# Kernel optimization log

Measured on AMD Instinct MI355X. Metric: run time of the kernel, lower is better.

The kernel has to match this reference:

```python
import jax, jax.numpy as jnp
import numpy as np

B, S, D, H = 1, 2048, 1024, 16
HD = D // H
DFF = 4 * D
EPS = 1e-5


def _layernorm(x, g, b):
    mu = jnp.mean(x, axis=-1, keepdims=True)
    var = jnp.mean(jnp.square(x - mu), axis=-1, keepdims=True)
    return (x - mu) * jax.lax.rsqrt(var + EPS) * g + b


def setup_inputs() -> dict:
    key = jax.random.key(0)
    ks = jax.random.split(key, 8)
    scale = 1.0 / np.sqrt(D)
    # standard ALiBi slopes: 2^(-8*i/H)
    slopes = jnp.asarray(2.0 ** (-8.0 * (np.arange(1, H + 1) / H)), dtype=jnp.float32)
    return {
        "x": jax.random.normal(ks[0], (B, S, D), jnp.float32),
        "alibi_slopes": slopes,
        "wq": jax.random.normal(ks[1], (D, D), jnp.float32) * scale,
        "wk": jax.random.normal(ks[2], (D, D), jnp.float32) * scale,
        "wv": jax.random.normal(ks[3], (D, D), jnp.float32) * scale,
        "wo": jax.random.normal(ks[4], (D, D), jnp.float32) * scale,
        "ff1_w": jax.random.normal(ks[5], (DFF, D), jnp.float32) * scale,
        "ff1_b": jnp.zeros((DFF,), jnp.float32),
        "ff2_w": jax.random.normal(ks[6], (D, DFF), jnp.float32) * (1.0 / np.sqrt(DFF)),
        "ff2_b": jnp.zeros((D,), jnp.float32),
        "ln1_g": jnp.ones((D,), jnp.float32),
        "ln1_b": jnp.zeros((D,), jnp.float32),
        "ln2_g": jnp.ones((D,), jnp.float32),
        "ln2_b": jnp.zeros((D,), jnp.float32),
    }


def reference(x, alibi_slopes, wq, wk, wv, wo, ff1_w, ff1_b, ff2_w, ff2_b,
              ln1_g, ln1_b, ln2_g, ln2_b):
    b, s, d = x.shape
    residual = x
    h = _layernorm(x, ln1_g, ln1_b)
    # projections (torch Linear: y = x @ W^T); split heads
    q = (h @ wq.T).reshape(b, s, H, HD)
    k = (h @ wk.T).reshape(b, s, H, HD)
    v = (h @ wv.T).reshape(b, s, H, HD)
    scores = jnp.einsum("bqhd,bkhd->bhqk", q, k) / np.sqrt(HD)  # [B,H,S,S]
    # ALiBi: distance[i,j] = j - i; scores -= slope * distance
    pos = jnp.arange(s, dtype=jnp.float32)
    dist = pos[None, :] - pos[:, None]                    # [S,S]
    scores = scores - alibi_slopes[None, :, None, None] * dist[None, None]
    # causal mask (query i attends to keys j <= i)
    causal = pos[:, None] >= pos[None, :]
    scores = jnp.where(causal[None, None], scores, -jnp.inf)
    attn = jax.nn.softmax(scores, axis=-1)
    out = jnp.einsum("bhqk,bkhd->bqhd", attn, v).reshape(b, s, d)
    out = out @ wo.T
    x = residual + out
    residual = x
    h2 = _layernorm(x, ln2_g, ln2_b)
    ff = jax.nn.gelu(h2 @ ff1_w.T + ff1_b, approximate=False) @ ff2_w.T + ff2_b
    return residual + ff
```

## Files before the change

kernel.cpp:

```cpp
#include <hip/hip_runtime.h>
#include <math.h>

typedef unsigned short u16;
typedef __bf16 bf16x8 __attribute__((ext_vector_type(8)));
typedef float f32x4 __attribute__((ext_vector_type(4)));
typedef u16 u16x4 __attribute__((ext_vector_type(4)));
typedef u16 u16x8 __attribute__((ext_vector_type(8)));

#define DEV __device__ __forceinline__

DEV u16 f2bf(float f) {
  unsigned u = __builtin_bit_cast(unsigned, f);
  u += 0x7FFFu + ((u >> 16) & 1u);
  return (u16)(u >> 16);
}
DEV float bf2f(u16 b) {
  unsigned u = ((unsigned)b) << 16;
  return __builtin_bit_cast(float, u);
}

DEV void gload16(const void* g, void* l) {
  __builtin_amdgcn_global_load_lds((__attribute__((address_space(1))) void*)g,
                                   (__attribute__((address_space(3))) void*)l, 16, 0, 0);
}

__launch_bounds__(256)
__global__ void cvt_all(const float* __restrict__ wq, const float* __restrict__ wk,
                        const float* __restrict__ wv, const float* __restrict__ wo,
                        const float* __restrict__ f1, const float* __restrict__ f2,
                        u16* __restrict__ dq, u16* __restrict__ dk, u16* __restrict__ dv,
                        u16* __restrict__ dwo, u16* __restrict__ df1, u16* __restrict__ df2) {
  int i = blockIdx.x * 256 + threadIdx.x;
  const float* src;
  u16* dst;
  int local;
  if (i < (1 << 18)) { src = wq; dst = dq; local = i; }
  else if (i < (2 << 18)) { src = wk; dst = dk; local = i - (1 << 18); }
  else if (i < (3 << 18)) { src = wv; dst = dv; local = i - (2 << 18); }
  else if (i < (4 << 18)) { src = wo; dst = dwo; local = i - (3 << 18); }
  else if (i < (4 << 18) + (1 << 20)) { src = f1; dst = df1; local = i - (4 << 18); }
  else { src = f2; dst = df2; local = i - ((4 << 18) + (1 << 20)); }
  float4 v = ((const float4*)src)[local];
  u16x4 o = { f2bf(v.x), f2bf(v.y), f2bf(v.z), f2bf(v.w) };
  ((u16x4*)dst)[local] = o;
}

__launch_bounds__(256)
__global__ void ln_rows(const float* __restrict__ x, const float* __restrict__ gam,
                        const float* __restrict__ bet, u16* __restrict__ out) {
  int row = blockIdx.x;
  int t = threadIdx.x;
  float4 v = ((const float4*)(x + (size_t)row * 1024))[t];
  float s = v.x + v.y + v.z + v.w;
  float s2 = v.x * v.x + v.y * v.y + v.z * v.z + v.w * v.w;
  for (int off = 1; off < 64; off <<= 1) {
    s += __shfl_xor(s, off);
    s2 += __shfl_xor(s2, off);
  }
  __shared__ float red[8];
  int wv = t >> 6, ln = t & 63;
  if (ln == 0) { red[wv] = s; red[wv + 4] = s2; }
  __syncthreads();
  s = red[0] + red[1] + red[2] + red[3];
  s2 = red[4] + red[5] + red[6] + red[7];
  float mu = s * (1.f / 1024.f);
  float var = s2 * (1.f / 1024.f) - mu * mu;
  float rs = rsqrtf(var + 1e-5f);
  float4 gv = ((const float4*)gam)[t];
  float4 bv = ((const float4*)bet)[t];
  u16x4 o = { f2bf((v.x - mu) * rs * gv.x + bv.x), f2bf((v.y - mu) * rs * gv.y + bv.y),
              f2bf((v.z - mu) * rs * gv.z + bv.z), f2bf((v.w - mu) * rs * gv.w + bv.w) };
  ((u16x4*)(out + (size_t)row * 1024))[t] = o;
}

__launch_bounds__(256)
__global__ void ln2_add(const float* __restrict__ x, const float* __restrict__ P0,
                        const float* __restrict__ P1, const float* __restrict__ gam,
                        const float* __restrict__ bet, float* __restrict__ x2,
                        u16* __restrict__ out) {
  int row = blockIdx.x;
  int t = threadIdx.x;
  size_t base = (size_t)row * 256 + t;
  float4 xv = ((const float4*)x)[base];
  float4 p0 = ((const float4*)P0)[base];
  float4 p1 = ((const float4*)P1)[base];
  float4 v = { xv.x + p0.x + p1.x, xv.y + p0.y + p1.y,
               xv.z + p0.z + p1.z, xv.w + p0.w + p1.w };
  ((float4*)x2)[base] = v;
  float s = v.x + v.y + v.z + v.w;
  float s2 = v.x * v.x + v.y * v.y + v.z * v.z + v.w * v.w;
  for (int off = 1; off < 64; off <<= 1) {
    s += __shfl_xor(s, off);
    s2 += __shfl_xor(s2, off);
  }
  __shared__ float red[8];
  int wv = t >> 6, ln = t & 63;
  if (ln == 0) { red[wv] = s; red[wv + 4] = s2; }
  __syncthreads();
  s = red[0] + red[1] + red[2] + red[3];
  s2 = red[4] + red[5] + red[6] + red[7];
  float mu = s * (1.f / 1024.f);
  float var = s2 * (1.f / 1024.f) - mu * mu;
  float rs = rsqrtf(var + 1e-5f);
  float4 gv = ((const float4*)gam)[t];
  float4 bv = ((const float4*)bet)[t];
  u16x4 o = { f2bf((v.x - mu) * rs * gv.x + bv.x), f2bf((v.y - mu) * rs * gv.y + bv.y),
              f2bf((v.z - mu) * rs * gv.z + bv.z), f2bf((v.w - mu) * rs * gv.w + bv.w) };
  ((u16x4*)(out + (size_t)row * 1024))[t] = o;
}

__launch_bounds__(256)
__global__ void final_add(const float* __restrict__ x2, const float* __restrict__ b2,
                          const u16* __restrict__ Q0, const u16* __restrict__ Q1,
                          float* __restrict__ out) {
  int row = blockIdx.x;
  int t = threadIdx.x;
  size_t base = (size_t)row * 256 + t;
  float4 xv = ((const float4*)x2)[base];
  float4 bv = ((const float4*)b2)[t];
  u16x4 q0 = ((const u16x4*)Q0)[base];
  u16x4 q1 = ((const u16x4*)Q1)[base];
  float4 o = { xv.x + bv.x + bf2f(q0[0]) + bf2f(q1[0]),
               xv.y + bv.y + bf2f(q0[1]) + bf2f(q1[1]),
               xv.z + bv.z + bf2f(q0[2]) + bf2f(q1[2]),
               xv.w + bv.w + bf2f(q0[3]) + bf2f(q1[3]) };
  ((float4*)out)[base] = o;
}

__launch_bounds__(256)
__global__ void transpose_v(const u16* __restrict__ V, u16* __restrict__ Vt) {
  const int st = blockIdx.x, h = blockIdx.y;
  __shared__ u16 tile[64][72];
  const int t = threadIdx.x;
  const int r = t >> 3, c8 = t & 7;
#pragma unroll
  for (int i = 0; i < 2; ++i) {
    int row = i * 32 + r;
    *(u16x8*)&tile[row][c8 * 8] =
        *(const u16x8*)&V[(size_t)(st * 64 + row) * 1024 + h * 64 + c8 * 8];
  }
  __syncthreads();
#pragma unroll
  for (int i = 0; i < 2; ++i) {
    int d = i * 32 + r;
    u16x8 o;
#pragma unroll
    for (int jj = 0; jj < 8; ++jj) o[jj] = tile[c8 * 8 + jj][d];
    *(u16x8*)&Vt[(size_t)(h * 64 + d) * 2048 + st * 64 + c8 * 8] = o;
  }
}

template <int BM, int BN, int WR, int WC, int EPI, int SPLITK, int SWZ>
__launch_bounds__(256, 2)
__global__ void gemm_bt(const u16* __restrict__ A, const u16* __restrict__ B,
                        void* __restrict__ C, const float* __restrict__ bias,
                        const float* __restrict__ resid, int M, int N, int K,
                        size_t zoff) {
  constexpr int FM = BM / WR / 16;
  constexpr int FN = BN / WC / 16;
  __shared__ u16 As[BM * 32];
  __shared__ u16 Bs[BN * 32];
  int bxi = blockIdx.x, byi = blockIdx.y, bzi = blockIdx.z;
  if constexpr (SWZ == 1) {
    int bid = bxi + 8 * (byi + (int)gridDim.y * bzi);
    int xcd = bid & 7, k = bid >> 3;
    bxi = xcd;
    byi = k % (int)gridDim.y;
    bzi = k / (int)gridDim.y;
  } else if constexpr (SWZ == 2) {
    int bid = bxi + 32 * byi;
    int xcd = bid & 7, k = bid >> 3;
    bxi = xcd * 4 + (k & 3);
    byi = k >> 2;
    bzi = 0;
  }
  const int t = threadIdx.x, lane = t & 63, w = t >> 6;
  const int wr = w / WC, wc = w % WC;
  const int g = lane >> 4, l16 = lane & 15;
  const int m0 = byi * BM, n0 = bxi * BN;
  const int ks = K / SPLITK;
  const int k0 = (SPLITK > 1) ? bzi * ks : 0;
  const size_t cbase = (SPLITK > 1) ? (size_t)bzi * zoff : 0;
  f32x4 acc[FM][FN] = {};
  const int nkt = ks >> 5;
  for (int kt = 0; kt < nkt; ++kt) {
    const u16* Ag = A + (size_t)m0 * K + k0 + kt * 32;
    const u16* Bg = B + (size_t)n0 * K + k0 + kt * 32;
#pragma unroll
    for (int i = 0; i < BM / 64; ++i) {
      int c = i * 256 + t;
      gload16(Ag + (size_t)(c >> 2) * K + (c & 3) * 8, &As[(i * 256 + w * 64) * 8]);
    }
#pragma unroll
    for (int i = 0; i < BN / 64; ++i) {
      int c = i * 256 + t;
      gload16(Bg + (size_t)(c >> 2) * K + (c & 3) * 8, &Bs[(i * 256 + w * 64) * 8]);
    }
    __syncthreads();
    bf16x8 af[FM], bfr[FN];
#pragma unroll
    for (int m = 0; m < FM; ++m)
      af[m] = *(const bf16x8*)&As[(wr * FM * 16 + m * 16 + l16) * 32 + g * 8];
#pragma unroll
    for (int n = 0; n < FN; ++n)
      bfr[n] = *(const bf16x8*)&Bs[(wc * FN * 16 + n * 16 + l16) * 32 + g * 8];
#pragma unroll
    for (int m = 0; m < FM; ++m)
#pragma unroll
      for (int n = 0; n < FN; ++n)
        acc[m][n] = __builtin_amdgcn_mfma_f32_16x16x32_bf16(af[m], bfr[n], acc[m][n], 0, 0, 0);
    __syncthreads();
  }
#pragma unroll
  for (int m = 0; m < FM; ++m)
#pragma unroll
    for (int n = 0; n < FN; ++n)
#pragma unroll
      for (int r = 0; r < 4; ++r) {
        int row = m0 + wr * FM * 16 + m * 16 + g * 4 + r;
        int col = n0 + wc * FN * 16 + n * 16 + l16;
        size_t idx = (size_t)row * N + col;
        float v = acc[m][n][r];
        if constexpr (EPI == 0) {
          ((u16*)C)[cbase + idx] = f2bf(v);
        } else if constexpr (EPI == 1) {
          v += bias[col];
          v = 0.5f * v * (1.f + erff(v * 0.70710678118f));
          ((u16*)C)[idx] = f2bf(v);
        } else if constexpr (EPI == 2) {
          ((float*)C)[idx] = v + bias[col] + resid[idx];
        } else if constexpr (EPI == 3) {
          ((float*)C)[idx] = v + resid[idx];
        } else {
          ((float*)C)[cbase + idx] = v;
        }
      }
}

__launch_bounds__(256, 2)
__global__ void gemm_qkv64(const u16* __restrict__ A, const u16* __restrict__ B0,
                           const u16* __restrict__ B1, const u16* __restrict__ B2,
                           u16* __restrict__ C0, u16* __restrict__ C1, u16* __restrict__ C2) {
  constexpr int FM = 4, FN = 2;
  const int K = 1024, N = 1024;
  int bid = blockIdx.x + 24 * blockIdx.y;
  int xcd = bid & 7, kk0 = bid >> 3;
  const int bxs = xcd * 3 + kk0 % 3;
  const int bys = kk0 / 3;
  const int which = bxs >> 3;
  const u16* B = which == 0 ? B0 : which == 1 ? B1 : B2;
  u16* C = which == 0 ? C0 : which == 1 ? C1 : C2;
  __shared__ u16 As[64 * 32];
  __shared__ u16 Bs[128 * 32];
  const int t = threadIdx.x, lane = t & 63, w = t >> 6;
  const int wc = w;
  const int g = lane >> 4, l16 = lane & 15;
  const int m0 = bys * 64, n0 = (bxs & 7) * 128;
  f32x4 acc[FM][FN] = {};
  for (int kt = 0; kt < 32; ++kt) {
    const u16* Ag = A + (size_t)m0 * K + kt * 32;
    const u16* Bg = B + (size_t)n0 * K + kt * 32;
    {
      int c = t;
      gload16(Ag + (size_t)(c >> 2) * K + (c & 3) * 8, &As[(w * 64) * 8]);
    }
#pragma unroll
    for (int i = 0; i < 2; ++i) {
      int c = i * 256 + t;
      gload16(Bg + (size_t)(c >> 2) * K + (c & 3) * 8, &Bs[(i * 256 + w * 64) * 8]);
    }
    __syncthreads();
    bf16x8 af[FM], bfr[FN];
#pragma unroll
    for (int m = 0; m < FM; ++m)
      af[m] = *(const bf16x8*)&As[(m * 16 + l16) * 32 + g * 8];
#pragma unroll
    for (int n = 0; n < FN; ++n)
      bfr[n] = *(const bf16x8*)&Bs[(wc * FN * 16 + n * 16 + l16) * 32 + g * 8];
#pragma unroll
    for (int m = 0; m < FM; ++m)
#pragma unroll
      for (int n = 0; n < FN; ++n)
        acc[m][n] = __builtin_amdgcn_mfma_f32_16x16x32_bf16(af[m], bfr[n], acc[m][n], 0, 0, 0);
    __syncthreads();
  }
#pragma unroll
  for (int m = 0; m < FM; ++m)
#pragma unroll
    for (int n = 0; n < FN; ++n)
#pragma unroll
      for (int r = 0; r < 4; ++r) {
        int row = m0 + m * 16 + g * 4 + r;
        int col = n0 + wc * FN * 16 + n * 16 + l16;
        C[(size_t)row * N + col] = f2bf(acc[m][n][r]);
      }
}

__launch_bounds__(512, 1)
__global__ void attn_fwd(const u16* __restrict__ Q, const u16* __restrict__ Kb,
                         const u16* __restrict__ Vt, const float* __restrict__ slopes,
                         u16* __restrict__ O) {
  const int bx = blockIdx.x;
  const int h = blockIdx.y;
  const int t = threadIdx.x, lane = t & 63, w8 = t >> 6;
  const int grp = w8 >> 2, w = w8 & 3;
  const int g = lane >> 4, l16 = lane & 15;
  const float slope = slopes[h];
  const int TA = bx + 1;
  const int qbB = 31 - bx;

  __shared__ u16 Ks[2][2][4096];
  __shared__ u16 Vs[2][2][4096];
  __shared__ u16 Ps[8][16][72];
  __shared__ float Bo[2][64][68];
  __shared__ float Bm[2][64], Bl[2][64];

  const int r0 = w * 8 + (lane >> 3), r1 = 32 + r0;
  const int c8 = lane & 7;
  const int c0s = c8 ^ (r0 & 7), c1s = c8 ^ (r1 & 7);
  const int sw = l16 & 7;

  auto stage = [&](int buf, int kv0) {
    gload16(Kb + (size_t)(kv0 + r0) * 1024 + h * 64 + c0s * 8, &Ks[grp][buf][(w * 64) * 8]);
    gload16(Kb + (size_t)(kv0 + r1) * 1024 + h * 64 + c1s * 8, &Ks[grp][buf][(256 + w * 64) * 8]);
    gload16(Vt + (size_t)(h * 64 + r0) * 2048 + kv0 + c0s * 8, &Vs[grp][buf][(w * 64) * 8]);
    gload16(Vt + (size_t)(h * 64 + r1) * 2048 + kv0 + c1s * 8, &Vs[grp][buf][(256 + w * 64) * 8]);
  };
  auto kvOf = [&](int idx) { return idx < TA ? idx * 64 : (idx - TA) * 64; };

  const int myStart = grp * 17;
  const int myEnd = grp == 0 ? 17 : 33;

  int qb = grp == 0 ? bx : qbB;
  int q0 = qb * 64 + w * 16;
  bf16x8 qf[2];
#pragma unroll
  for (int kk = 0; kk < 2; ++kk)
    qf[kk] = *(const bf16x8*)&Q[(size_t)(q0 + l16) * 1024 + h * 64 + kk * 32 + g * 8];
  f32x4 o_acc[4] = {};
  float m_run[4], l_run[4];
#pragma unroll
  for (int r = 0; r < 4; ++r) { m_run[r] = -1e30f; l_run[r] = 0.f; }

  stage(0, kvOf(myStart));
  __syncthreads();

  int cur = 0;
  for (int it = 0; it < 17; ++it) {
    const int idx = myStart + it;
    const bool active = idx < myEnd;
    if (grp == 0 && idx == TA) {
#pragma unroll
      for (int d = 0; d < 4; ++d)
#pragma unroll
        for (int r = 0; r < 4; ++r) {
          int row = q0 + g * 4 + r;
          O[(size_t)row * 1024 + h * 64 + d * 16 + l16] = f2bf(o_acc[d][r] / l_run[r]);
        }
      qb = qbB;
      q0 = qb * 64 + w * 16;
#pragma unroll
      for (int kk = 0; kk < 2; ++kk)
        qf[kk] = *(const bf16x8*)&Q[(size_t)(q0 + l16) * 1024 + h * 64 + kk * 32 + g * 8];
#pragma unroll
      for (int d = 0; d < 4; ++d) o_acc[d] = f32x4{};
#pragma unroll
      for (int r = 0; r < 4; ++r) { m_run[r] = -1e30f; l_run[r] = 0.f; }
    }
    if (idx + 1 < myEnd) stage(cur ^ 1, kvOf(idx + 1));
    if (active) {
      const int kv0 = kvOf(idx);
      const bool lastT = (idx == TA - 1) || (idx == 32);
      f32x4 s[4];
      __builtin_amdgcn_s_setprio(1);
#pragma unroll
      for (int n = 0; n < 4; ++n) {
        bf16x8 kf0 = *(const bf16x8*)&Ks[grp][cur][(n * 16 + l16) * 64 + ((g ^ sw) * 8)];
        bf16x8 kf1 = *(const bf16x8*)&Ks[grp][cur][(n * 16 + l16) * 64 + (((4 + g) ^ sw) * 8)];
        f32x4 z = {};
        s[n] = __builtin_amdgcn_mfma_f32_16x16x32_bf16(qf[0], kf0, z, 0, 0, 0);
        s[n] = __builtin_amdgcn_mfma_f32_16x16x32_bf16(qf[1], kf1, s[n], 0, 0, 0);
      }
      __builtin_amdgcn_s_setprio(0);
      float sv[4][4];
      float mtile[4] = { -1e30f, -1e30f, -1e30f, -1e30f };
      const float aB = -slope * (float)(kv0 + l16);
#pragma unroll
      for (int n = 0; n < 4; ++n) {
        const float aN = aB - slope * (float)(n * 16);
        const int kj = kv0 + n * 16 + l16;
#pragma unroll
        for (int r = 0; r < 4; ++r) {
          float val = fmaf(s[n][r], 0.125f, aN);
          if (lastT) {
            int qi = q0 + g * 4 + r;
            val = (kj <= qi) ? val : -1e30f;
          }
          sv[n][r] = val;
          mtile[r] = fmaxf(mtile[r], val);
        }
      }
#pragma unroll
      for (int r = 0; r < 4; ++r) {
        float v = mtile[r];
        v = fmaxf(v, __shfl_xor(v, 1));
        v = fmaxf(v, __shfl_xor(v, 2));
        v = fmaxf(v, __shfl_xor(v, 4));
        v = fmaxf(v, __shfl_xor(v, 8));
        mtile[r] = v;
      }
      float sc[4];
#pragma unroll
      for (int r = 0; r < 4; ++r) {
        float mnew = fmaxf(m_run[r], mtile[r]);
        sc[r] = __expf(m_run[r] - mnew);
        m_run[r] = mnew;
      }
      float tsum[4] = { 0.f, 0.f, 0.f, 0.f };
#pragma unroll
      for (int n = 0; n < 4; ++n)
#pragma unroll
        for (int r = 0; r < 4; ++r) {
          float p = __expf(sv[n][r] - m_run[r]);
          sv[n][r] = p;
          tsum[r] += p;
        }
#pragma unroll
      for (int r = 0; r < 4; ++r) {
        float v = tsum[r];
        v += __shfl_xor(v, 1);
        v += __shfl_xor(v, 2);
        v += __shfl_xor(v, 4);
        v += __shfl_xor(v, 8);
        l_run[r] = l_run[r] * sc[r] + v;
      }
#pragma unroll
      for (int d = 0; d < 4; ++d)
#pragma unroll
        for (int r = 0; r < 4; ++r) o_acc[d][r] *= sc[r];
#pragma unroll
      for (int n = 0; n < 4; ++n)
#pragma unroll
        for (int r = 0; r < 4; ++r)
          Ps[w8][g * 4 + r][n * 16 + l16] = f2bf(sv[n][r]);
      bf16x8 pf[2];
#pragma unroll
      for (int kk = 0; kk < 2; ++kk)
        pf[kk] = *(const bf16x8*)&Ps[w8][l16][kk * 32 + g * 8];
      __builtin_amdgcn_s_setprio(1);
#pragma unroll
      for (int d = 0; d < 4; ++d) {
#pragma unroll
        for (int kk = 0; kk < 2; ++kk) {
          bf16x8 vv = *(const bf16x8*)&Vs[grp][cur][(d * 16 + l16) * 64 + (((kk * 4 + g) ^ sw) * 8)];
          o_acc[d] = __builtin_amdgcn_mfma_f32_16x16x32_bf16(pf[kk], vv, o_acc[d], 0, 0, 0);
        }
      }
      __builtin_amdgcn_s_setprio(0);
    }
    __syncthreads();
    cur ^= 1;
  }
#pragma unroll
  for (int d = 0; d < 4; ++d)
#pragma unroll
    for (int r = 0; r < 4; ++r)
      Bo[grp][w * 16 + g * 4 + r][d * 16 + l16] = o_acc[d][r];
  if (l16 == 0) {
#pragma unroll
    for (int r = 0; r < 4; ++r) {
      Bm[grp][w * 16 + g * 4 + r] = m_run[r];
      Bl[grp][w * 16 + g * 4 + r] = l_run[r];
    }
  }
  __syncthreads();
  if (grp == 0) {
#pragma unroll
    for (int rr = 0; rr < 4; ++rr) {
      const int row = w * 16 + g * 4 + rr;
      float m0 = Bm[0][row], m1 = Bm[1][row];
      float mm = fmaxf(m0, m1);
      float w0 = __expf(m0 - mm), w1 = __expf(m1 - mm);
      float ll = Bl[0][row] * w0 + Bl[1][row] * w1;
      float inv = 1.f / ll;
#pragma unroll
      for (int d = 0; d < 4; ++d) {
        int col = d * 16 + l16;
        float o = Bo[0][row][col] * w0 + Bo[1][row][col] * w1;
        O[(size_t)(qbB * 64 + row) * 1024 + h * 64 + col] = f2bf(o * inv);
      }
    }
  }
}

extern "C" void kernel_launch(void* const* d_in, const int* in_sizes, int n_in,
                              void* d_out, int out_size, void* d_ws, size_t ws_size,
                              hipStream_t stream) {
  const float* x = (const float*)d_in[0];
  const float* slopes = (const float*)d_in[1];
  const float* wq = (const float*)d_in[2];
  const float* wk = (const float*)d_in[3];
  const float* wv = (const float*)d_in[4];
  const float* wo = (const float*)d_in[5];
  const float* ff1w = (const float*)d_in[6];
  const float* ff1b = (const float*)d_in[7];
  const float* ff2w = (const float*)d_in[8];
  const float* ff2b = (const float*)d_in[9];
  const float* ln1g = (const float*)d_in[10];
  const float* ln1b = (const float*)d_in[11];
  const float* ln2g = (const float*)d_in[12];
  const float* ln2b = (const float*)d_in[13];
  float* out = (float*)d_out;

  if (ws_size < (size_t)(56u << 20)) return;

  char* ws = (char*)d_ws;
  u16* hbuf = (u16*)(ws + 0);
  u16* Qb = (u16*)(ws + (4u << 20));
  u16* Kbf = (u16*)(ws + (8u << 20));
  u16* Vbf = (u16*)(ws + (12u << 20));
  u16* Vtb = (u16*)(ws + (16u << 20));
  float* P0 = (float*)(ws + (4u << 20));
  float* P1 = (float*)(ws + (12u << 20));
  u16* ffact = Qb;
  float* x2 = (float*)(ws + (20u << 20));
  u16* h2 = (u16*)(ws + (28u << 20));
  u16* Q1p = h2;
  u16* wqb = (u16*)(ws + (32u << 20));
  u16* wkb = (u16*)(ws + (34u << 20));
  u16* wvb = (u16*)(ws + (36u << 20));
  u16* wob = (u16*)(ws + (38u << 20));
  u16* ff1wb = (u16*)(ws + (40u << 20));
  u16* ff2wb = (u16*)(ws + (48u << 20));
  u16* attnO = hbuf;
  u16* Q0p = hbuf;
  const size_t q1off = (size_t)(28u << 20) / 2;

  cvt_all<<<12288, 256, 0, stream>>>(wq, wk, wv, wo, ff1w, ff2w,
                                     wqb, wkb, wvb, wob, ff1wb, ff2wb);

  ln_rows<<<2048, 256, 0, stream>>>(x, ln1g, ln1b, hbuf);
  gemm_qkv64<<<dim3(24, 32), 256, 0, stream>>>(hbuf, wqb, wkb, wvb, Qb, Kbf, Vbf);
  transpose_v<<<dim3(32, 16), 256, 0, stream>>>(Vbf, Vtb);
  attn_fwd<<<dim3(16, 16), 512, 0, stream>>>(Qb, Kbf, Vtb, slopes, attnO);
  gemm_bt<64, 128, 1, 4, 4, 2, 1><<<dim3(8, 32, 2), 256, 0, stream>>>(
      attnO, wob, P0, nullptr, nullptr, 2048, 1024, 1024, (size_t)2048 * 1024);
  ln2_add<<<2048, 256, 0, stream>>>(x, P0, P1, ln2g, ln2b, x2, h2);
  gemm_bt<128, 128, 2, 2, 1, 1, 2><<<dim3(32, 16), 256, 0, stream>>>(
      h2, ff1wb, ffact, ff1b, nullptr, 2048, 4096, 1024, 0);
  gemm_bt<64, 128, 1, 4, 0, 2, 1><<<dim3(8, 32, 2), 256, 0, stream>>>(
      ffact, ff2wb, Q0p, nullptr, nullptr, 2048, 1024, 4096, q1off);
  final_add<<<2048, 256, 0, stream>>>(x2, ff2b, Q0p, Q1p, out);
}
```

Before: 191.3 us.

## Split attention blocks across grid z and merge partials in separate kernel

The 512-thread attention block that held two wave groups sharing LDS is split into two independent 256-thread blocks along grid z. Each writes its partial output plus running max and sum to global workspace, and a new merge kernel combines the two partials for the second query block. The aim is more, smaller blocks with less LDS each, so several blocks can share a CU (launch bounds 256,4). In exchange it adds a kernel launch and a global round trip for the partials. Separately, the weight conversion and first layernorm kernels are fused into one launch.

```diff
diff --git a/kernel.cpp b/kernel.cpp
--- a/kernel.cpp
+++ b/kernel.cpp
@@ -25,52 +25,52 @@
 }
 
 __launch_bounds__(256)
-__global__ void cvt_all(const float* __restrict__ wq, const float* __restrict__ wk,
-                        const float* __restrict__ wv, const float* __restrict__ wo,
-                        const float* __restrict__ f1, const float* __restrict__ f2,
-                        u16* __restrict__ dq, u16* __restrict__ dk, u16* __restrict__ dv,
-                        u16* __restrict__ dwo, u16* __restrict__ df1, u16* __restrict__ df2) {
-  int i = blockIdx.x * 256 + threadIdx.x;
-  const float* src;
-  u16* dst;
-  int local;
-  if (i < (1 << 18)) { src = wq; dst = dq; local = i; }
-  else if (i < (2 << 18)) { src = wk; dst = dk; local = i - (1 << 18); }
-  else if (i < (3 << 18)) { src = wv; dst = dv; local = i - (2 << 18); }
-  else if (i < (4 << 18)) { src = wo; dst = dwo; local = i - (3 << 18); }
-  else if (i < (4 << 18) + (1 << 20)) { src = f1; dst = df1; local = i - (4 << 18); }
-  else { src = f2; dst = df2; local = i - ((4 << 18) + (1 << 20)); }
-  float4 v = ((const float4*)src)[local];
-  u16x4 o = { f2bf(v.x), f2bf(v.y), f2bf(v.z), f2bf(v.w) };
-  ((u16x4*)dst)[local] = o;
-}
-
-__launch_bounds__(256)
-__global__ void ln_rows(const float* __restrict__ x, const float* __restrict__ gam,
-                        const float* __restrict__ bet, u16* __restrict__ out) {
-  int row = blockIdx.x;
+__global__ void prep(const float* __restrict__ x, const float* __restrict__ gam,
+                     const float* __restrict__ bet, u16* __restrict__ hout,
+                     const float* __restrict__ wq, const float* __restrict__ wk,
+                     const float* __restrict__ wv, const float* __restrict__ wo,
+                     const float* __restrict__ f1, const float* __restrict__ f2,
+                     u16* __restrict__ dq, u16* __restrict__ dk, u16* __restrict__ dv,
+                     u16* __restrict__ dwo, u16* __restrict__ df1, u16* __restrict__ df2) {
   int t = threadIdx.x;
-  float4 v = ((const float4*)(x + (size_t)row * 1024))[t];
-  float s = v.x + v.y + v.z + v.w;
-  float s2 = v.x * v.x + v.y * v.y + v.z * v.z + v.w * v.w;
-  for (int off = 1; off < 64; off <<= 1) {
-    s += __shfl_xor(s, off);
-    s2 += __shfl_xor(s2, off);
-  }
-  __shared__ float red[8];
-  int wv = t >> 6, ln = t & 63;
-  if (ln == 0) { red[wv] = s; red[wv + 4] = s2; }
-  __syncthreads();
-  s = red[0] + red[1] + red[2] + red[3];
-  s2 = red[4] + red[5] + red[6] + red[7];
-  float mu = s * (1.f / 1024.f);
-  float var = s2 * (1.f / 1024.f) - mu * mu;
-  float rs = rsqrtf(var + 1e-5f);
-  float4 gv = ((const float4*)gam)[t];
-  float4 bv = ((const float4*)bet)[t];
-  u16x4 o = { f2bf((v.x - mu) * rs * gv.x + bv.x), f2bf((v.y - mu) * rs * gv.y + bv.y),
-              f2bf((v.z - mu) * rs * gv.z + bv.z), f2bf((v.w - mu) * rs * gv.w + bv.w) };
-  ((u16x4*)(out + (size_t)row * 1024))[t] = o;
+  if (blockIdx.x < 2048) {
+    int row = blockIdx.x;
+    float4 v = ((const float4*)(x + (size_t)row * 1024))[t];
+    float s = v.x + v.y + v.z + v.w;
+    float s2 = v.x * v.x + v.y * v.y + v.z * v.z + v.w * v.w;
+    for (int off = 1; off < 64; off <<= 1) {
+      s += __shfl_xor(s, off);
+      s2 += __shfl_xor(s2, off);
+    }
+    __shared__ float red[8];
+    int wv0 = t >> 6, ln = t & 63;
+    if (ln == 0) { red[wv0] = s; red[wv0 + 4] = s2; }
+    __syncthreads();
+    s = red[0] + red[1] + red[2] + red[3];
+    s2 = red[4] + red[5] + red[6] + red[7];
+    float mu = s * (1.f / 1024.f);
+    float var = s2 * (1.f / 1024.f) - mu * mu;
+    float rs = rsqrtf(var + 1e-5f);
+    float4 gv = ((const float4*)gam)[t];
+    float4 bv = ((const float4*)bet)[t];
+    u16x4 o = { f2bf((v.x - mu) * rs * gv.x + bv.x), f2bf((v.y - mu) * rs * gv.y + bv.y),
+                f2bf((v.z - mu) * rs * gv.z + bv.z), f2bf((v.w - mu) * rs * gv.w + bv.w) };
+    ((u16x4*)(hout + (size_t)row * 1024))[t] = o;
+  } else {
+    int i = (blockIdx.x - 2048) * 256 + t;
+    const float* src;
+    u16* dst;
+    int local;
+    if (i < (1 << 18)) { src = wq; dst = dq; local = i; }
+    else if (i < (2 << 18)) { src = wk; dst = dk; local = i - (1 << 18); }
+    else if (i < (3 << 18)) { src = wv; dst = dv; local = i - (2 << 18); }
+    else if (i < (4 << 18)) { src = wo; dst = dwo; local = i - (3 << 18); }
+    else if (i < (4 << 18) + (1 << 20)) { src = f1; dst = df1; local = i - (4 << 18); }
+    else { src = f2; dst = df2; local = i - ((4 << 18) + (1 << 20)); }
+    float4 v = ((const float4*)src)[local];
+    u16x4 o = { f2bf(v.x), f2bf(v.y), f2bf(v.z), f2bf(v.w) };
+    ((u16x4*)dst)[local] = o;
+  }
 }
 
 __launch_bounds__(256)
@@ -296,24 +296,23 @@
       }
 }
 
-__launch_bounds__(512, 1)
+__launch_bounds__(256, 4)
 __global__ void attn_fwd(const u16* __restrict__ Q, const u16* __restrict__ Kb,
                          const u16* __restrict__ Vt, const float* __restrict__ slopes,
-                         u16* __restrict__ O) {
-  const int bx = blockIdx.x;
+                         u16* __restrict__ O, float* __restrict__ BoG,
+                         float* __restrict__ BmlG) {
+  const int p = blockIdx.x;
   const int h = blockIdx.y;
-  const int t = threadIdx.x, lane = t & 63, w8 = t >> 6;
-  const int grp = w8 >> 2, w = w8 & 3;
+  const int z = blockIdx.z;
+  const int t = threadIdx.x, lane = t & 63, w = t >> 6;
   const int g = lane >> 4, l16 = lane & 15;
   const float slope = slopes[h];
-  const int TA = bx + 1;
-  const int qbB = 31 - bx;
-
-  __shared__ u16 Ks[2][2][4096];
-  __shared__ u16 Vs[2][2][4096];
-  __shared__ u16 Ps[8][16][72];
-  __shared__ float Bo[2][64][68];
-  __shared__ float Bm[2][64], Bl[2][64];
+  const int TA = p + 1;
+  const int qbB = 31 - p;
+
+  __shared__ u16 Ks[2][4096];
+  __shared__ u16 Vs[2][4096];
+  __shared__ u16 Ps[4][16][72];
 
   const int r0 = w * 8 + (lane >> 3), r1 = 32 + r0;
   const int c8 = lane & 7;
@@ -321,17 +320,17 @@
   const int sw = l16 & 7;
 
   auto stage = [&](int buf, int kv0) {
-    gload16(Kb + (size_t)(kv0 + r0) * 1024 + h * 64 + c0s * 8, &Ks[grp][buf][(w * 64) * 8]);
-    gload16(Kb + (size_t)(kv0 + r1) * 1024 + h * 64 + c1s * 8, &Ks[grp][buf][(256 + w * 64) * 8]);
-    gload16(Vt + (size_t)(h * 64 + r0) * 2048 + kv0 + c0s * 8, &Vs[grp][buf][(w * 64) * 8]);
-    gload16(Vt + (size_t)(h * 64 + r1) * 2048 + kv0 + c1s * 8, &Vs[grp][buf][(256 + w * 64) * 8]);
+    gload16(Kb + (size_t)(kv0 + r0) * 1024 + h * 64 + c0s * 8, &Ks[buf][(w * 64) * 8]);
+    gload16(Kb + (size_t)(kv0 + r1) * 1024 + h * 64 + c1s * 8, &Ks[buf][(256 + w * 64) * 8]);
+    gload16(Vt + (size_t)(h * 64 + r0) * 2048 + kv0 + c0s * 8, &Vs[buf][(w * 64) * 8]);
+    gload16(Vt + (size_t)(h * 64 + r1) * 2048 + kv0 + c1s * 8, &Vs[buf][(256 + w * 64) * 8]);
   };
   auto kvOf = [&](int idx) { return idx < TA ? idx * 64 : (idx - TA) * 64; };
 
-  const int myStart = grp * 17;
-  const int myEnd = grp == 0 ? 17 : 33;
-
-  int qb = grp == 0 ? bx : qbB;
+  const int myStart = z * 17;
+  const int myEnd = z ? 33 : 17;
+
+  int qb = (z == 0) ? p : qbB;
   int q0 = qb * 64 + w * 16;
   bf16x8 qf[2];
 #pragma unroll
@@ -349,7 +348,7 @@
   for (int it = 0; it < 17; ++it) {
     const int idx = myStart + it;
     const bool active = idx < myEnd;
-    if (grp == 0 && idx == TA) {
+    if (z == 0 && idx == TA) {
 #pragma unroll
       for (int d = 0; d < 4; ++d)
 #pragma unroll
@@ -375,10 +374,10 @@
       __builtin_amdgcn_s_setprio(1);
 #pragma unroll
       for (int n = 0; n < 4; ++n) {
-        bf16x8 kf0 = *(const bf16x8*)&Ks[grp][cur][(n * 16 + l16) * 64 + ((g ^ sw) * 8)];
-        bf16x8 kf1 = *(const bf16x8*)&Ks[grp][cur][(n * 16 + l16) * 64 + (((4 + g) ^ sw) * 8)];
-        f32x4 z = {};
-        s[n] = __builtin_amdgcn_mfma_f32_16x16x32_bf16(qf[0], kf0, z, 0, 0, 0);
+        bf16x8 kf0 = *(const bf16x8*)&Ks[cur][(n * 16 + l16) * 64 + ((g ^ sw) * 8)];
+        bf16x8 kf1 = *(const bf16x8*)&Ks[cur][(n * 16 + l16) * 64 + (((4 + g) ^ sw) * 8)];
+        f32x4 z4 = {};
+        s[n] = __builtin_amdgcn_mfma_f32_16x16x32_bf16(qf[0], kf0, z4, 0, 0, 0);
         s[n] = __builtin_amdgcn_mfma_f32_16x16x32_bf16(qf[1], kf1, s[n], 0, 0, 0);
       }
       __builtin_amdgcn_s_setprio(0);
@@ -421,9 +420,9 @@
       for (int n = 0; n < 4; ++n)
 #pragma unroll
         for (int r = 0; r < 4; ++r) {
-          float p = __expf(sv[n][r] - m_run[r]);
-          sv[n][r] = p;
-          tsum[r] += p;
+          float pp = __expf(sv[n][r] - m_run[r]);
+          sv[n][r] = pp;
+          tsum[r] += pp;
         }
 #pragma unroll
       for (int r = 0; r < 4; ++r) {
@@ -442,17 +441,17 @@
       for (int n = 0; n < 4; ++n)
 #pragma unroll
         for (int r = 0; r < 4; ++r)
-          Ps[w8][g * 4 + r][n * 16 + l16] = f2bf(sv[n][r]);
+          Ps[w][g * 4 + r][n * 16 + l16] = f2bf(sv[n][r]);
       bf16x8 pf[2];
 #pragma unroll
       for (int kk = 0; kk < 2; ++kk)
-        pf[kk] = *(const bf16x8*)&Ps[w8][l16][kk * 32 + g * 8];
+        pf[kk] = *(const bf16x8*)&Ps[w][l16][kk * 32 + g * 8];
       __builtin_amdgcn_s_setprio(1);
 #pragma unroll
       for (int d = 0; d < 4; ++d) {
 #pragma unroll
         for (int kk = 0; kk < 2; ++kk) {
-          bf16x8 vv = *(const bf16x8*)&Vs[grp][cur][(d * 16 + l16) * 64 + (((kk * 4 + g) ^ sw) * 8)];
+          bf16x8 vv = *(const bf16x8*)&Vs[cur][(d * 16 + l16) * 64 + (((kk * 4 + g) ^ sw) * 8)];
           o_acc[d] = __builtin_amdgcn_mfma_f32_16x16x32_bf16(pf[kk], vv, o_acc[d], 0, 0, 0);
         }
       }
@@ -461,35 +460,48 @@
     __syncthreads();
     cur ^= 1;
   }
+  const size_t slot = ((size_t)p * 16 + h) * 2 + z;
+  float* Bo = BoG + slot * 4096;
+  float* Bml = BmlG + slot * 128;
 #pragma unroll
   for (int d = 0; d < 4; ++d)
 #pragma unroll
     for (int r = 0; r < 4; ++r)
-      Bo[grp][w * 16 + g * 4 + r][d * 16 + l16] = o_acc[d][r];
+      Bo[(w * 16 + g * 4 + r) * 64 + d * 16 + l16] = o_acc[d][r];
   if (l16 == 0) {
 #pragma unroll
     for (int r = 0; r < 4; ++r) {
-      Bm[grp][w * 16 + g * 4 + r] = m_run[r];
-      Bl[grp][w * 16 + g * 4 + r] = l_run[r];
-    }
-  }
-  __syncthreads();
-  if (grp == 0) {
-#pragma unroll
-    for (int rr = 0; rr < 4; ++rr) {
-      const int row = w * 16 + g * 4 + rr;
-      float m0 = Bm[0][row], m1 = Bm[1][row];
-      float mm = fmaxf(m0, m1);
-      float w0 = __expf(m0 - mm), w1 = __expf(m1 - mm);
-      float ll = Bl[0][row] * w0 + Bl[1][row] * w1;
-      float inv = 1.f / ll;
-#pragma unroll
-      for (int d = 0; d < 4; ++d) {
-        int col = d * 16 + l16;
-        float o = Bo[0][row][col] * w0 + Bo[1][row][col] * w1;
-        O[(size_t)(qbB * 64 + row) * 1024 + h * 64 + col] = f2bf(o * inv);
-      }
-    }
+      Bml[w * 16 + g * 4 + r] = m_run[r];
+      Bml[64 + w * 16 + g * 4 + r] = l_run[r];
+    }
+  }
+}
+
+__launch_bounds__(256)
+__global__ void merge_b(const float* __restrict__ BoG, const float* __restrict__ BmlG,
+                        u16* __restrict__ O) {
+  const int p = blockIdx.x, h = blockIdx.y;
+  const int qbB = 31 - p;
+  const size_t s0 = (((size_t)p * 16 + h) * 2 + 0);
+  const size_t s1 = s0 + 1;
+  const float* Bo0 = BoG + s0 * 4096;
+  const float* Bo1 = BoG + s1 * 4096;
+  const float* Bml0 = BmlG + s0 * 128;
+  const float* Bml1 = BmlG + s1 * 128;
+  const int t = threadIdx.x;
+#pragma unroll
+  for (int i = 0; i < 4; ++i) {
+    int idx = t + i * 256;
+    int row = idx >> 4, c4 = idx & 15;
+    float m0 = Bml0[row], m1 = Bml1[row];
+    float mm = fmaxf(m0, m1);
+    float w0 = __expf(m0 - mm), w1 = __expf(m1 - mm);
+    float inv = 1.f / (Bml0[64 + row] * w0 + Bml1[64 + row] * w1);
+    float4 a = ((const float4*)Bo0)[(size_t)row * 16 + c4];
+    float4 b = ((const float4*)Bo1)[(size_t)row * 16 + c4];
+    u16x4 o = { f2bf((a.x * w0 + b.x * w1) * inv), f2bf((a.y * w0 + b.y * w1) * inv),
+                f2bf((a.z * w0 + b.z * w1) * inv), f2bf((a.w * w0 + b.w * w1) * inv) };
+    *(u16x4*)&O[(size_t)(qbB * 64 + row) * 1024 + h * 64 + c4 * 4] = o;
   }
 }
 
@@ -524,7 +536,9 @@
   float* P1 = (float*)(ws + (12u << 20));
   u16* ffact = Qb;
   float* x2 = (float*)(ws + (20u << 20));
+  float* BoG = (float*)(ws + (20u << 20));
   u16* h2 = (u16*)(ws + (28u << 20));
+  float* BmlG = (float*)(ws + (28u << 20));
   u16* Q1p = h2;
   u16* wqb = (u16*)(ws + (32u << 20));
   u16* wkb = (u16*)(ws + (34u << 20));
@@ -536,13 +550,12 @@
   u16* Q0p = hbuf;
   const size_t q1off = (size_t)(28u << 20) / 2;
 
-  cvt_all<<<12288, 256, 0, stream>>>(wq, wk, wv, wo, ff1w, ff2w,
-                                     wqb, wkb, wvb, wob, ff1wb, ff2wb);
-
-  ln_rows<<<2048, 256, 0, stream>>>(x, ln1g, ln1b, hbuf);
+  prep<<<2048 + 12288, 256, 0, stream>>>(x, ln1g, ln1b, hbuf, wq, wk, wv, wo, ff1w, ff2w,
+                                         wqb, wkb, wvb, wob, ff1wb, ff2wb);
   gemm_qkv64<<<dim3(24, 32), 256, 0, stream>>>(hbuf, wqb, wkb, wvb, Qb, Kbf, Vbf);
   transpose_v<<<dim3(32, 16), 256, 0, stream>>>(Vbf, Vtb);
-  attn_fwd<<<dim3(16, 16), 512, 0, stream>>>(Qb, Kbf, Vtb, slopes, attnO);
+  attn_fwd<<<dim3(16, 16, 2), 256, 0, stream>>>(Qb, Kbf, Vtb, slopes, attnO, BoG, BmlG);
+  merge_b<<<dim3(16, 16), 256, 0, stream>>>(BoG, BmlG, attnO);
   gemm_bt<64, 128, 1, 4, 4, 2, 1><<<dim3(8, 32, 2), 256, 0, stream>>>(
       attnO, wob, P0, nullptr, nullptr, 2048, 1024, 1024, (size_t)2048 * 1024);
   ln2_add<<<2048, 256, 0, stream>>>(x, P0, P1, ln2g, ln2b, x2, h2);
```

Result: no change. 189.9 us (-0.7%).
